# Performance work log

Measured on AMD Instinct MI355X. Metric: run time of the kernel, lower is better.

Reference implementation:

```python
import jax, jax.numpy as jnp
import numpy as np

DT = 0.01


def _mlp(x, W1, b1, W2, b2, W3, b3):
    # Linear -> tanh -> Linear -> tanh -> Linear
    h = jnp.tanh(x @ W1 + b1)
    h = jnp.tanh(h @ W2 + b2)
    return h @ W3 + b3


def setup_inputs() -> dict:
    B, T, D, H, F = 512, 128, 512, 1024, 128
    key = jax.random.key(0)
    ks = jax.random.split(key, 20)

    def lin(kw, kb, fan_in, fan_out):
        W = jax.random.normal(kw, (fan_in, fan_out), jnp.float32) / jnp.sqrt(jnp.float32(fan_in))
        b = jnp.zeros((fan_out,), jnp.float32)
        return W, b

    window = jax.random.normal(ks[0], (B, T, D), jnp.float32)
    eW1, eb1 = lin(ks[1], ks[2], D, H)
    eW2, eb2 = lin(ks[3], ks[4], H, H)
    eW3, eb3 = lin(ks[5], ks[6], H, F)
    dW1, db1 = lin(ks[7], ks[8], F, H)
    dW2, db2 = lin(ks[9], ks[10], H, H)
    dW3, db3 = lin(ks[11], ks[12], H, D)
    kW1, kb1 = lin(ks[13], ks[14], F, F)  # koopman_dim -> 2*num_eigenvalues == F
    kW2, kb2 = lin(ks[15], ks[16], F, F)
    return {
        'window': window,
        'eW1': eW1, 'eb1': eb1, 'eW2': eW2, 'eb2': eb2, 'eW3': eW3, 'eb3': eb3,
        'dW1': dW1, 'db1': db1, 'dW2': dW2, 'db2': db2, 'dW3': dW3, 'db3': db3,
        'kW1': kW1, 'kb1': kb1, 'kW2': kW2, 'kb2': kb2,
    }


def _koopman(z0, T, kW1, kb1, kW2, kb2):
    # parameterization: Linear -> tanh -> Linear, producing (mu, omega) per eigen-pair
    B, F = z0.shape
    n_eig = F // 2
    p = jnp.tanh(z0 @ kW1 + kb1) @ kW2 + kb2          # [B, 2*n_eig]
    p = p.reshape(B, n_eig, 2)
    mu, omega = p[..., 0], p[..., 1]
    exp_mu = jnp.exp(mu * DT)
    c = jnp.cos(omega * DT)
    s = jnp.sin(omega * DT)
    # per-sample 2x2 rotation-scaling blocks: [B, n_eig, 2, 2]
    blocks = jnp.stack([
        jnp.stack([exp_mu * c, -exp_mu * s], axis=-1),
        jnp.stack([exp_mu * s, exp_mu * c], axis=-1),
    ], axis=-2)

    def step(z, _):
        zp = z.reshape(B, n_eig, 2)
        zn = jnp.einsum('bnij,bnj->bni', blocks, zp).reshape(B, F)
        return zn, zn

    _, preds = jax.lax.scan(step, z0, None, length=T)  # [T, B, F]
    return jnp.transpose(preds, (1, 0, 2))             # [B, T, F]


def reference(window, eW1, eb1, eW2, eb2, eW3, eb3,
              dW1, db1, dW2, db2, dW3, db3,
              kW1, kb1, kW2, kb2):
    x0 = window[:, 0, :]          # [B, D]
    targets = window[:, 1:, :]    # [B, T-1, D]
    T = targets.shape[1]

    z0 = _mlp(x0, eW1, eb1, eW2, eb2, eW3, eb3)          # [B, F]
    x0_recon = _mlp(z0, dW1, db1, dW2, db2, dW3, db3)    # [B, D]
    z_pred = _koopman(z0, T, kW1, kb1, kW2, kb2)         # [B, T-1, F]
    x_pred = _mlp(z_pred, dW1, db1, dW2, db2, dW3, db3)  # [B, T-1, D]
    z_true = _mlp(targets, eW1, eb1, eW2, eb2, eW3, eb3) # [B, T-1, F]

    loss_recon = jnp.mean((x0_recon - x0) ** 2)
    loss_linear = jnp.mean((z_pred - z_true) ** 2)
    loss_pred = jnp.mean((x_pred - targets) ** 2)
    total = loss_recon + loss_linear + loss_pred
    return total, loss_recon, loss_linear, loss_pred
```

## Files before the change

### kernel.cpp

```cpp
#include <hip/hip_runtime.h>
#include <cstddef>
#include <cstdint>


#define KDT 0.01f
#define CH 16384
#define NCHUNK 4

typedef _Float16 f16;
typedef f16 f16x8 __attribute__((ext_vector_type(8)));
typedef f16 f16x4 __attribute__((ext_vector_type(4)));
typedef float f32x4 __attribute__((ext_vector_type(4)));

typedef __attribute__((address_space(1))) const unsigned int gu32;
typedef __attribute__((address_space(3))) unsigned int lu32;

__device__ __forceinline__ void gl_lds16(const void* g, void* l) {
    __builtin_amdgcn_global_load_lds((gu32*)g, (lu32*)l, 16, 0, 0);
}

__device__ __forceinline__ float fast_tanh(float x) {
    x = fminf(fmaxf(x, -15.f), 15.f);
    const float e = __expf(2.f * x);
    return (e - 1.f) / (e + 1.f);
}

#define PB_LIN 0
#define PB_REC 4096
#define PB_PRED 6144
#define PB_TOTAL 8192

template <int MODE, bool TANH, bool OUTF16>
__global__ __launch_bounds__(256) void k_gemm_f16(const f16* __restrict__ A,
                                                  const f16* __restrict__ Wt,
                                                  const float* __restrict__ bias,
                                                  void* __restrict__ Cv,
                                                  int M, int N, int K,
                                                  const float* __restrict__ win,
                                                  int g0,
                                                  double* __restrict__ p0,
                                                  double* __restrict__ p1)
{
    __shared__ __align__(16) f16 As[128][32];
    __shared__ __align__(16) f16 Bs[128][32];
    __shared__ double sm[256];

    const int t  = threadIdx.x;
    const int l  = t & 63;
    const int wv = t >> 6;
    const int wr = wv >> 1, wc = wv & 1;
    const int lm = l & 15, lk = l >> 4;

    const int gx = gridDim.x;
    const int nwg = gx * gridDim.y;
    const int orig = blockIdx.y * gx + blockIdx.x;
    int tile = orig;
    if ((nwg & 7) == 0) tile = (orig & 7) * (nwg >> 3) + (orig >> 3);
    const int bm = tile / gx;
    const int bn = tile % gx;

    const f16* Ab = A  + (size_t)bm * 128 * K;
    const f16* Bb = Wt + (size_t)bn * 128 * K;
    char* sA = (char*)&As[0][0];
    char* sB = (char*)&Bs[0][0];

    const int rswz = (lm >> 1) & 3;
    const int rdA = (lk ^ rswz) * 16;

    f32x4 acc[4][4] = {};

    for (int k0 = 0; k0 < K; k0 += 32) {
#pragma unroll
        for (int r = 0; r < 2; ++r) {
            const int c = r * 256 + t;
            const int row = c >> 2;
            const int sslot = (c & 3) ^ ((row >> 1) & 3);
            const size_t goff = (size_t)row * K + (size_t)k0 + (size_t)sslot * 8;
            gl_lds16(Ab + goff, sA + (size_t)c * 16);
            gl_lds16(Bb + goff, sB + (size_t)c * 16);
        }
        __syncthreads();

        f16x8 af[4], bf[4];
#pragma unroll
        for (int i = 0; i < 4; ++i) {
            af[i] = *reinterpret_cast<const f16x8*>(sA + (wr * 64 + i * 16 + lm) * 64 + rdA);
            bf[i] = *reinterpret_cast<const f16x8*>(sB + (wc * 64 + i * 16 + lm) * 64 + rdA);
        }
#pragma unroll
        for (int i = 0; i < 4; ++i)
#pragma unroll
            for (int j = 0; j < 4; ++j)
                acc[i][j] = __builtin_amdgcn_mfma_f32_16x16x32_f16(af[i], bf[j], acc[i][j], 0, 0, 0);
        __syncthreads();
    }

    const int col0 = bn * 128 + wc * 64;

    if (MODE == 0) {
        const int row0 = bm * 128 + wr * 64;
#pragma unroll
        for (int j = 0; j < 4; ++j) {
            const int col = col0 + j * 16 + lm;
            const float bv = bias[col];
#pragma unroll
            for (int i = 0; i < 4; ++i)
#pragma unroll
                for (int q = 0; q < 4; ++q) {
                    const int row = row0 + i * 16 + lk * 4 + q;
                    float v = acc[i][j][q] + bv;
                    if (TANH) v = fast_tanh(v);
                    if (OUTF16) ((f16*)Cv)[(size_t)row * N + col] = (f16)v;
                    else        ((float*)Cv)[(size_t)row * N + col] = v;
                }
        }
    } else {
        double s0 = 0.0, s1 = 0.0;
#pragma unroll
        for (int i = 0; i < 4; ++i) {
#pragma unroll
            for (int q = 0; q < 4; ++q) {
                const int rl = bm * 128 + wr * 64 + i * 16 + lk * 4 + q;
                const int g  = g0 + rl;
                const int tt = g & 127;
#pragma unroll
                for (int j = 0; j < 4; ++j) {
                    const int col = col0 + j * 16 + lm;
                    const float v = acc[i][j][q] + bias[col];
                    const float d = v - win[(size_t)g * 512 + col];
                    if (tt == 0) s0 += (double)d * d;
                    else         s1 += (double)d * d;
                }
            }
        }
        sm[t] = s0;
        __syncthreads();
        for (int o = 128; o > 0; o >>= 1) {
            if (t < o) sm[t] += sm[t + o];
            __syncthreads();
        }
        if (t == 0) p0[tile] = sm[0];
        __syncthreads();
        sm[t] = s1;
        __syncthreads();
        for (int o = 128; o > 0; o >>= 1) {
            if (t < o) sm[t] += sm[t + o];
            __syncthreads();
        }
        if (t == 0) p1[tile] = sm[0];
    }
}

__global__ __launch_bounds__(256) void k_wt(const float* __restrict__ W,
                                            f16* __restrict__ Wt, int K, int N)
{
    __shared__ float tl[32][33];
    const int n0 = blockIdx.x * 32, k0 = blockIdx.y * 32;
    const int tx = threadIdx.x & 31, ty = threadIdx.x >> 5;
#pragma unroll
    for (int i = 0; i < 32; i += 8)
        tl[ty + i][tx] = W[(size_t)(k0 + ty + i) * N + n0 + tx];
    __syncthreads();
#pragma unroll
    for (int i = 0; i < 32; i += 8)
        Wt[(size_t)(n0 + ty + i) * K + k0 + tx] = (f16)tl[tx][ty + i];
}

__global__ __launch_bounds__(256) void k_gather_all(const float* __restrict__ win,
                                                    f16* __restrict__ out, int g0)
{
    const int i = blockIdx.x * 256 + threadIdx.x;
    if (i >= CH * 64) return;
    const int r = i >> 6, c8 = i & 63;
    const float* s = win + ((size_t)(g0 + r)) * 512 + c8 * 8;
    const float4 v0 = *reinterpret_cast<const float4*>(s);
    const float4 v1 = *reinterpret_cast<const float4*>(s + 4);
    f16x8 o;
    o[0] = (f16)v0.x; o[1] = (f16)v0.y; o[2] = (f16)v0.z; o[3] = (f16)v0.w;
    o[4] = (f16)v1.x; o[5] = (f16)v1.y; o[6] = (f16)v1.z; o[7] = (f16)v1.w;
    *reinterpret_cast<f16x8*>(out + (size_t)r * 512 + c8 * 8) = o;
}

__global__ __launch_bounds__(256) void k_gather_z0(const float* __restrict__ cZfull,
                                                   float* __restrict__ z0f32,
                                                   f16* __restrict__ z0f16)
{
    const int i = blockIdx.x * 256 + threadIdx.x;
    if (i >= 512 * 32) return;
    const int b = i >> 5, c4 = i & 31;
    const float4 v = *reinterpret_cast<const float4*>(cZfull + (size_t)b * 16384 + c4 * 4);
    *reinterpret_cast<float4*>(z0f32 + (size_t)b * 128 + c4 * 4) = v;
    f16x4 o;
    o[0] = (f16)v.x; o[1] = (f16)v.y; o[2] = (f16)v.z; o[3] = (f16)v.w;
    *reinterpret_cast<f16x4*>(z0f16 + (size_t)b * 128 + c4 * 4) = o;
}

__global__ __launch_bounds__(256) void k_koop(const float* __restrict__ cZ,
                                              const float* __restrict__ z0,
                                              const float* __restrict__ pK,
                                              int g0,
                                              f16* __restrict__ decin,
                                              double* __restrict__ p0)
{
    const int idx = blockIdx.x * 256 + threadIdx.x;
    const int r = idx >> 4, c8 = idx & 15;
    const int g = g0 + r;
    const int tt = g & 127;
    const int bb = g >> 7;

    float zt[8];
    *reinterpret_cast<float4*>(zt)     = *reinterpret_cast<const float4*>(cZ + (size_t)r * 128 + c8 * 8);
    *reinterpret_cast<float4*>(zt + 4) = *reinterpret_cast<const float4*>(cZ + (size_t)r * 128 + c8 * 8 + 4);

    double s = 0.0;
    float ov[8];
    if (tt == 0) {
#pragma unroll
        for (int k = 0; k < 8; ++k) ov[k] = zt[k];
    } else {
        float zz[8], qq[8];
        *reinterpret_cast<float4*>(zz)     = *reinterpret_cast<const float4*>(z0 + (size_t)bb * 128 + c8 * 8);
        *reinterpret_cast<float4*>(zz + 4) = *reinterpret_cast<const float4*>(z0 + (size_t)bb * 128 + c8 * 8 + 4);
        *reinterpret_cast<float4*>(qq)     = *reinterpret_cast<const float4*>(pK + (size_t)bb * 128 + c8 * 8);
        *reinterpret_cast<float4*>(qq + 4) = *reinterpret_cast<const float4*>(pK + (size_t)bb * 128 + c8 * 8 + 4);
        const float tf = KDT * (float)tt;
#pragma unroll
        for (int pr = 0; pr < 4; ++pr) {
            const float e = __expf(qq[2 * pr] * tf);
            float sn, cs;
            __sincosf(qq[2 * pr + 1] * tf, &sn, &cs);
            const float zx = zz[2 * pr], zy = zz[2 * pr + 1];
            const float a = e * (cs * zx - sn * zy);
            const float b = e * (sn * zx + cs * zy);
            ov[2 * pr] = a; ov[2 * pr + 1] = b;
            const float d0 = a - zt[2 * pr], d1 = b - zt[2 * pr + 1];
            s += (double)d0 * d0 + (double)d1 * d1;
        }
    }
    f16x8 o;
#pragma unroll
    for (int k = 0; k < 8; ++k) o[k] = (f16)ov[k];
    *reinterpret_cast<f16x8*>(decin + (size_t)r * 128 + c8 * 8) = o;

    __shared__ double sm[256];
    sm[threadIdx.x] = s;
    __syncthreads();
    for (int off = 128; off > 0; off >>= 1) {
        if (threadIdx.x < (unsigned)off) sm[threadIdx.x] += sm[threadIdx.x + off];
        __syncthreads();
    }
    if (threadIdx.x == 0) p0[blockIdx.x] = sm[0];
}

__global__ __launch_bounds__(256) void k_finalize(const double* __restrict__ pb,
                                                  float* __restrict__ out)
{
    __shared__ double sm[256];
    const int t = threadIdx.x;
    double a0 = 0.0, a1 = 0.0, a2 = 0.0;
    for (int i = t; i < 4096; i += 256) a0 += pb[PB_LIN + i];
    for (int i = t; i < 2048; i += 256) a1 += pb[PB_REC + i];
    for (int i = t; i < 2048; i += 256) a2 += pb[PB_PRED + i];

    double r[3];
    double v[3] = {a0, a1, a2};
    for (int k = 0; k < 3; ++k) {
        sm[t] = v[k];
        __syncthreads();
        for (int o = 128; o > 0; o >>= 1) {
            if (t < o) sm[t] += sm[t + o];
            __syncthreads();
        }
        r[k] = sm[0];
        __syncthreads();
    }
    if (t == 0) {
        const double linear = r[0] / (65024.0 * 128.0);
        const double recon  = r[1] / (512.0 * 512.0);
        const double pred   = r[2] / (65024.0 * 512.0);
        out[0] = (float)(recon + linear + pred);
        out[1] = (float)recon;
        out[2] = (float)linear;
        out[3] = (float)pred;
    }
}

extern "C" void kernel_launch(void* const* d_in, const int* in_sizes, int n_in,
                              void* d_out, int out_size, void* d_ws, size_t ws_size,
                              hipStream_t stream)
{
    const float* window = (const float*)d_in[0];
    const float* eW1 = (const float*)d_in[1];
    const float* eb1 = (const float*)d_in[2];
    const float* eW2 = (const float*)d_in[3];
    const float* eb2 = (const float*)d_in[4];
    const float* eW3 = (const float*)d_in[5];
    const float* eb3 = (const float*)d_in[6];
    const float* dW1 = (const float*)d_in[7];
    const float* db1 = (const float*)d_in[8];
    const float* dW2 = (const float*)d_in[9];
    const float* db2 = (const float*)d_in[10];
    const float* dW3 = (const float*)d_in[11];
    const float* db3 = (const float*)d_in[12];
    const float* kW1 = (const float*)d_in[13];
    const float* kb1 = (const float*)d_in[14];
    const float* kW2 = (const float*)d_in[15];
    const float* kb2 = (const float*)d_in[16];
    float* out = (float*)d_out;
    (void)in_sizes; (void)n_in; (void)out_size; (void)ws_size;

    char* p = (char*)d_ws;
    size_t off = 0;
    auto takeB = [&](size_t bytes) -> char* {
        char* r = p + off;
        off += (bytes + 255) & ~(size_t)255;
        return r;
    };
    double* pb = (double*)takeB(PB_TOTAL * 8);
    f16* eW1t = (f16*)takeB((size_t)512 * 1024 * 2);
    f16* eW2t = (f16*)takeB((size_t)1024 * 1024 * 2);
    f16* eW3t = (f16*)takeB((size_t)1024 * 128 * 2);
    f16* dW1t = (f16*)takeB((size_t)128 * 1024 * 2);
    f16* dW2t = (f16*)takeB((size_t)1024 * 1024 * 2);
    f16* dW3t = (f16*)takeB((size_t)1024 * 512 * 2);
    f16* kW1t = (f16*)takeB((size_t)128 * 128 * 2);
    f16* kW2t = (f16*)takeB((size_t)128 * 128 * 2);
    float* z0f32 = (float*)takeB((size_t)65536 * 4);
    f16* z0f16 = (f16*)takeB((size_t)65536 * 2);
    f16* hK = (f16*)takeB((size_t)65536 * 2);
    float* pKbuf = (float*)takeB((size_t)65536 * 4);
    float* cZfull = (float*)takeB((size_t)65536 * 128 * 4);
    f16* cIn = (f16*)takeB((size_t)CH * 512 * 2);
    f16* cH1 = (f16*)takeB((size_t)CH * 1024 * 2);
    f16* cH2 = (f16*)takeB((size_t)CH * 1024 * 2);
    f16* decin = (f16*)takeB((size_t)CH * 128 * 2);

    hipMemsetAsync(pb, 0, PB_TOTAL * 8, stream);

    auto G = [&](const f16* A, const f16* Wt, const float* b, void* C,
                 int M, int N, int K, bool tanh_, bool f16out) {
        dim3 grid(N / 128, M / 128);
        if (tanh_)       k_gemm_f16<0, true,  true ><<<grid, 256, 0, stream>>>(A, Wt, b, C, M, N, K, nullptr, 0, nullptr, nullptr);
        else if (f16out) k_gemm_f16<0, false, true ><<<grid, 256, 0, stream>>>(A, Wt, b, C, M, N, K, nullptr, 0, nullptr, nullptr);
        else             k_gemm_f16<0, false, false><<<grid, 256, 0, stream>>>(A, Wt, b, C, M, N, K, nullptr, 0, nullptr, nullptr);
    };
    auto WT = [&](const float* W, f16* Wt, int K, int N) {
        k_wt<<<dim3(N / 32, K / 32), 256, 0, stream>>>(W, Wt, K, N);
    };

    WT(eW1, eW1t, 512, 1024);  WT(eW2, eW2t, 1024, 1024); WT(eW3, eW3t, 1024, 128);
    WT(dW1, dW1t, 128, 1024);  WT(dW2, dW2t, 1024, 1024); WT(dW3, dW3t, 1024, 512);
    WT(kW1, kW1t, 128, 128);   WT(kW2, kW2t, 128, 128);

    for (int c = 0; c < NCHUNK; ++c) {
        const int g0 = c * CH;
        k_gather_all<<<CH * 64 / 256, 256, 0, stream>>>(window, cIn, g0);
        G(cIn, eW1t, eb1, cH1, CH, 1024, 512, true, true);
        G(cH1, eW2t, eb2, cH2, CH, 1024, 1024, true, true);
        G(cH2, eW3t, eb3, cZfull + (size_t)g0 * 128, CH, 128, 1024, false, false);
    }

    k_gather_z0<<<64, 256, 0, stream>>>(cZfull, z0f32, z0f16);
    G(z0f16, kW1t, kb1, hK, 512, 128, 128, true, true);
    G(hK,    kW2t, kb2, pKbuf, 512, 128, 128, false, false);

    for (int c = 0; c < NCHUNK; ++c) {
        const int g0 = c * CH;
        k_koop<<<CH * 16 / 256, 256, 0, stream>>>(cZfull + (size_t)g0 * 128, z0f32, pKbuf,
                                                  g0, decin, pb + PB_LIN + c * 1024);
        G(decin, dW1t, db1, cH1, CH, 1024, 128, true, true);
        G(cH1,   dW2t, db2, cH2, CH, 1024, 1024, true, true);
        k_gemm_f16<2, false, false><<<dim3(4, CH / 128), 256, 0, stream>>>(
            cH2, dW3t, db3, nullptr, CH, 512, 1024,
            window, g0, pb + PB_REC + c * 512, pb + PB_PRED + c * 512);
    }

    k_finalize<<<1, 256, 0, stream>>>(pb, out);
}
```

Measured before the change: 1.197 ms.

## Double GEMM K-tile to 64, template N/K, and drop chunking when workspace allows

The GEMM kernel now stages 64-wide K tiles in LDS (two MFMA sub-steps per barrier pair) with an 8-slot XOR swizzle, halving the number of sync points per K. N and K become compile-time template parameters so address arithmetic and loop bounds are constant. The host runs the whole batch in one chunk instead of four when the workspace is large enough, which cuts launch count and gives larger grids. The trade-offs are doubled LDS per block, which may lower occupancy, and a larger workspace requirement.

```diff
diff --git a/kernel.cpp b/kernel.cpp
--- a/kernel.cpp
+++ b/kernel.cpp
@@ -4,8 +4,6 @@
 
 
 #define KDT 0.01f
-#define CH 16384
-#define NCHUNK 4
 
 typedef _Float16 f16;
 typedef f16 f16x8 __attribute__((ext_vector_type(8)));
@@ -30,20 +28,19 @@
 #define PB_PRED 6144
 #define PB_TOTAL 8192
 
-template <int MODE, bool TANH, bool OUTF16>
+template <int MODE, bool TANH, bool OUTF16, int N, int K>
 __global__ __launch_bounds__(256) void k_gemm_f16(const f16* __restrict__ A,
                                                   const f16* __restrict__ Wt,
                                                   const float* __restrict__ bias,
                                                   void* __restrict__ Cv,
-                                                  int M, int N, int K,
+                                                  int M,
                                                   const float* __restrict__ win,
                                                   int g0,
                                                   double* __restrict__ p0,
                                                   double* __restrict__ p1)
 {
-    __shared__ __align__(16) f16 As[128][32];
-    __shared__ __align__(16) f16 Bs[128][32];
-    __shared__ double sm[256];
+    __shared__ __align__(16) f16 As[128][64];
+    __shared__ __align__(16) f16 Bs[128][64];
 
     const int t  = threadIdx.x;
     const int l  = t & 63;
@@ -64,34 +61,37 @@
     char* sA = (char*)&As[0][0];
     char* sB = (char*)&Bs[0][0];
 
-    const int rswz = (lm >> 1) & 3;
-    const int rdA = (lk ^ rswz) * 16;
+    const int rswz = lm & 7;
 
     f32x4 acc[4][4] = {};
 
-    for (int k0 = 0; k0 < K; k0 += 32) {
-#pragma unroll
-        for (int r = 0; r < 2; ++r) {
+    for (int k0 = 0; k0 < K; k0 += 64) {
+#pragma unroll
+        for (int r = 0; r < 4; ++r) {
             const int c = r * 256 + t;
-            const int row = c >> 2;
-            const int sslot = (c & 3) ^ ((row >> 1) & 3);
-            const size_t goff = (size_t)row * K + (size_t)k0 + (size_t)sslot * 8;
+            const int row = c >> 3;
+            const int sl = (c & 7) ^ (row & 7);
+            const size_t goff = (size_t)row * K + (size_t)k0 + (size_t)sl * 8;
             gl_lds16(Ab + goff, sA + (size_t)c * 16);
             gl_lds16(Bb + goff, sB + (size_t)c * 16);
         }
         __syncthreads();
 
-        f16x8 af[4], bf[4];
-#pragma unroll
-        for (int i = 0; i < 4; ++i) {
-            af[i] = *reinterpret_cast<const f16x8*>(sA + (wr * 64 + i * 16 + lm) * 64 + rdA);
-            bf[i] = *reinterpret_cast<const f16x8*>(sB + (wc * 64 + i * 16 + lm) * 64 + rdA);
-        }
-#pragma unroll
-        for (int i = 0; i < 4; ++i)
-#pragma unroll
-            for (int j = 0; j < 4; ++j)
-                acc[i][j] = __builtin_amdgcn_mfma_f32_16x16x32_f16(af[i], bf[j], acc[i][j], 0, 0, 0);
+#pragma unroll
+        for (int ks = 0; ks < 2; ++ks) {
+            const int rd = ((ks * 4 + lk) ^ rswz) * 16;
+            f16x8 af[4], bf[4];
+#pragma unroll
+            for (int i = 0; i < 4; ++i) {
+                af[i] = *reinterpret_cast<const f16x8*>(sA + (wr * 64 + i * 16 + lm) * 128 + rd);
+                bf[i] = *reinterpret_cast<const f16x8*>(sB + (wc * 64 + i * 16 + lm) * 128 + rd);
+            }
+#pragma unroll
+            for (int i = 0; i < 4; ++i)
+#pragma unroll
+                for (int j = 0; j < 4; ++j)
+                    acc[i][j] = __builtin_amdgcn_mfma_f32_16x16x32_f16(af[i], bf[j], acc[i][j], 0, 0, 0);
+        }
         __syncthreads();
     }
 
@@ -115,6 +115,7 @@
                 }
         }
     } else {
+        __shared__ double sm[256];
         double s0 = 0.0, s1 = 0.0;
 #pragma unroll
         for (int i = 0; i < 4; ++i) {
@@ -167,10 +168,10 @@
 }
 
 __global__ __launch_bounds__(256) void k_gather_all(const float* __restrict__ win,
-                                                    f16* __restrict__ out, int g0)
+                                                    f16* __restrict__ out, int g0, int nrows)
 {
     const int i = blockIdx.x * 256 + threadIdx.x;
-    if (i >= CH * 64) return;
+    if (i >= nrows * 64) return;
     const int r = i >> 6, c8 = i & 63;
     const float* s = win + ((size_t)(g0 + r)) * 512 + c8 * 8;
     const float4 v0 = *reinterpret_cast<const float4*>(s);
@@ -307,7 +308,10 @@
     const float* kW2 = (const float*)d_in[15];
     const float* kb2 = (const float*)d_in[16];
     float* out = (float*)d_out;
-    (void)in_sizes; (void)n_in; (void)out_size; (void)ws_size;
+    (void)in_sizes; (void)n_in; (void)out_size;
+
+    const int nch = (ws_size >= (420ull << 20)) ? 1 : 4;
+    const int MC  = 65536 / nch;
 
     char* p = (char*)d_ws;
     size_t off = 0;
@@ -330,20 +334,13 @@
     f16* hK = (f16*)takeB((size_t)65536 * 2);
     float* pKbuf = (float*)takeB((size_t)65536 * 4);
     float* cZfull = (float*)takeB((size_t)65536 * 128 * 4);
-    f16* cIn = (f16*)takeB((size_t)CH * 512 * 2);
-    f16* cH1 = (f16*)takeB((size_t)CH * 1024 * 2);
-    f16* cH2 = (f16*)takeB((size_t)CH * 1024 * 2);
-    f16* decin = (f16*)takeB((size_t)CH * 128 * 2);
+    f16* cIn  = (f16*)takeB((size_t)MC * 512 * 2);
+    f16* cH1  = (f16*)takeB((size_t)MC * 1024 * 2);
+    f16* cH2  = (f16*)takeB((size_t)MC * 1024 * 2);
+    f16* decin = (f16*)takeB((size_t)MC * 128 * 2);
 
     hipMemsetAsync(pb, 0, PB_TOTAL * 8, stream);
 
-    auto G = [&](const f16* A, const f16* Wt, const float* b, void* C,
-                 int M, int N, int K, bool tanh_, bool f16out) {
-        dim3 grid(N / 128, M / 128);
-        if (tanh_)       k_gemm_f16<0, true,  true ><<<grid, 256, 0, stream>>>(A, Wt, b, C, M, N, K, nullptr, 0, nullptr, nullptr);
-        else if (f16out) k_gemm_f16<0, false, true ><<<grid, 256, 0, stream>>>(A, Wt, b, C, M, N, K, nullptr, 0, nullptr, nullptr);
-        else             k_gemm_f16<0, false, false><<<grid, 256, 0, stream>>>(A, Wt, b, C, M, N, K, nullptr, 0, nullptr, nullptr);
-    };
     auto WT = [&](const float* W, f16* Wt, int K, int N) {
         k_wt<<<dim3(N / 32, K / 32), 256, 0, stream>>>(W, Wt, K, N);
     };
@@ -352,27 +349,34 @@
     WT(dW1, dW1t, 128, 1024);  WT(dW2, dW2t, 1024, 1024); WT(dW3, dW3t, 1024, 512);
     WT(kW1, kW1t, 128, 128);   WT(kW2, kW2t, 128, 128);
 
-    for (int c = 0; c < NCHUNK; ++c) {
-        const int g0 = c * CH;
-        k_gather_all<<<CH * 64 / 256, 256, 0, stream>>>(window, cIn, g0);
-        G(cIn, eW1t, eb1, cH1, CH, 1024, 512, true, true);
-        G(cH1, eW2t, eb2, cH2, CH, 1024, 1024, true, true);
-        G(cH2, eW3t, eb3, cZfull + (size_t)g0 * 128, CH, 128, 1024, false, false);
+    for (int c = 0; c < nch; ++c) {
+        const int g0 = c * MC;
+        k_gather_all<<<MC * 64 / 256, 256, 0, stream>>>(window, cIn, g0, MC);
+        k_gemm_f16<0, true, true, 1024, 512><<<dim3(8, MC / 128), 256, 0, stream>>>(
+            cIn, eW1t, eb1, cH1, MC, nullptr, 0, nullptr, nullptr);
+        k_gemm_f16<0, true, true, 1024, 1024><<<dim3(8, MC / 128), 256, 0, stream>>>(
+            cH1, eW2t, eb2, cH2, MC, nullptr, 0, nullptr, nullptr);
+        k_gemm_f16<0, false, false, 128, 1024><<<dim3(1, MC / 128), 256, 0, stream>>>(
+            cH2, eW3t, eb3, cZfull + (size_t)g0 * 128, MC, nullptr, 0, nullptr, nullptr);
     }
 
     k_gather_z0<<<64, 256, 0, stream>>>(cZfull, z0f32, z0f16);
-    G(z0f16, kW1t, kb1, hK, 512, 128, 128, true, true);
-    G(hK,    kW2t, kb2, pKbuf, 512, 128, 128, false, false);
-
-    for (int c = 0; c < NCHUNK; ++c) {
-        const int g0 = c * CH;
-        k_koop<<<CH * 16 / 256, 256, 0, stream>>>(cZfull + (size_t)g0 * 128, z0f32, pKbuf,
-                                                  g0, decin, pb + PB_LIN + c * 1024);
-        G(decin, dW1t, db1, cH1, CH, 1024, 128, true, true);
-        G(cH1,   dW2t, db2, cH2, CH, 1024, 1024, true, true);
-        k_gemm_f16<2, false, false><<<dim3(4, CH / 128), 256, 0, stream>>>(
-            cH2, dW3t, db3, nullptr, CH, 512, 1024,
-            window, g0, pb + PB_REC + c * 512, pb + PB_PRED + c * 512);
+    k_gemm_f16<0, true, true, 128, 128><<<dim3(1, 4), 256, 0, stream>>>(
+        z0f16, kW1t, kb1, hK, 512, nullptr, 0, nullptr, nullptr);
+    k_gemm_f16<0, false, false, 128, 128><<<dim3(1, 4), 256, 0, stream>>>(
+        hK, kW2t, kb2, pKbuf, 512, nullptr, 0, nullptr, nullptr);
+
+    for (int c = 0; c < nch; ++c) {
+        const int g0 = c * MC;
+        k_koop<<<MC / 16, 256, 0, stream>>>(cZfull + (size_t)g0 * 128, z0f32, pKbuf,
+                                            g0, decin, pb + PB_LIN + (g0 >> 4));
+        k_gemm_f16<0, true, true, 1024, 128><<<dim3(8, MC / 128), 256, 0, stream>>>(
+            decin, dW1t, db1, cH1, MC, nullptr, 0, nullptr, nullptr);
+        k_gemm_f16<0, true, true, 1024, 1024><<<dim3(8, MC / 128), 256, 0, stream>>>(
+            cH1, dW2t, db2, cH2, MC, nullptr, 0, nullptr, nullptr);
+        k_gemm_f16<2, false, false, 512, 1024><<<dim3(4, MC / 128), 256, 0, stream>>>(
+            cH2, dW3t, db3, nullptr, MC,
+            window, g0, pb + PB_REC + (g0 >> 5), pb + PB_PRED + (g0 >> 5));
     }
 
     k_finalize<<<1, 256, 0, stream>>>(pb, out);
```

New measurement: 1.040 ms. -13.1%, faster.
